# Kernel optimization log

Hardware: AMD Instinct MI355X
Metric: run time of the kernel (lower is better)

The kernel has to match this reference:

```python
import jax, jax.numpy as jnp
import numpy as np

GAMMA = 12.0
EMB_INIT = 0.05


def setup_inputs() -> dict:
    key = jax.random.key(0)
    k1, k2, k3 = jax.random.split(key, 3)
    num_chunks, chunk_size, neg_sample_size, hidden_dim = 4, 512, 256, 512
    heads = jax.random.normal(k1, (num_chunks * chunk_size, hidden_dim), dtype=jnp.float32)
    relations = jax.random.normal(k2, (num_chunks * chunk_size, hidden_dim // 2), dtype=jnp.float32)
    tails = jax.random.normal(k3, (num_chunks * neg_sample_size, hidden_dim), dtype=jnp.float32)
    return {
        "heads": heads,
        "relations": relations,
        "tails": tails,
        "num_chunks": num_chunks,
        "chunk_size": chunk_size,
        "neg_sample_size": neg_sample_size,
    }


def reference(heads, relations, tails, num_chunks, chunk_size, neg_sample_size):
    # RotatE tail-negative scoring (create_neg with neg_head=False)
    hidden_dim = heads.shape[1]
    h = hidden_dim // 2
    re_head, im_head = heads[:, :h], heads[:, h:]
    # rotate head by relation phase
    phase_rel = relations / (EMB_INIT / np.pi)
    rel_real, rel_imag = jnp.cos(phase_rel), jnp.sin(phase_rel)
    real = re_head * rel_real - im_head * rel_imag  # [nc*cs, h]
    imag = re_head * rel_imag + im_head * rel_real
    # broadcast subtract against negative tails
    tmp_r = real.reshape(num_chunks, chunk_size, 1, h)
    tmp_i = imag.reshape(num_chunks, chunk_size, 1, h)
    tails4 = tails.reshape(num_chunks, 1, neg_sample_size, hidden_dim)
    t_r, t_i = tails4[..., :h], tails4[..., h:]
    dr = tmp_r - t_r  # [nc, cs, ns, h]
    di = tmp_i - t_i
    score = jnp.sqrt(dr * dr + di * di).sum(-1)  # [nc, cs, ns]
    return GAMMA - score
```

## Files before the change

kernel.cpp:

```cpp
#include <hip/hip_runtime.h>

#define NC 4
#define CS 512
#define NS 256
#define HD 512
#define H  256
#define GAMMA_F 12.0f
#define PHASE_SCALE 62.83185307179586477f

#define TI 32
#define TJ 32
#define KT 32

__global__ __launch_bounds__(256) void score_kernel(
    const float* __restrict__ heads,
    const float* __restrict__ relations,
    const float* __restrict__ tails,
    float* __restrict__ out)
{
    __shared__ float hr[TI][KT + 1];
    __shared__ float hi_[TI][KT + 1];
    __shared__ float tr[TJ][KT + 1];
    __shared__ float ti_[TJ][KT + 1];

    int bid = blockIdx.x;
    int c = bid >> 7;
    int rem = bid & 127;
    int hTile = rem >> 3;
    int tTile = rem & 7;
    int hBase = c * CS + hTile * TI;
    int tBase = c * NS + tTile * TJ;

    int tid = threadIdx.x;
    int tx = tid & 15;
    int ty = tid >> 4;

    int lr = tid >> 3;
    int lk = (tid & 7) * 4;

    float acc00 = 0.f, acc01 = 0.f, acc10 = 0.f, acc11 = 0.f;

    for (int k0 = 0; k0 < H; k0 += KT) {
        const float* hp = heads + (size_t)(hBase + lr) * HD + k0 + lk;
        float4 hre = *reinterpret_cast<const float4*>(hp);
        float4 him = *reinterpret_cast<const float4*>(hp + H);
        float4 rel = *reinterpret_cast<const float4*>(
            relations + (size_t)(hBase + lr) * H + k0 + lk);
        const float* tp = tails + (size_t)(tBase + lr) * HD + k0 + lk;
        float4 tre = *reinterpret_cast<const float4*>(tp);
        float4 tim = *reinterpret_cast<const float4*>(tp + H);

        __syncthreads();

        {
            float s, cc;
            __sincosf(rel.x * PHASE_SCALE, &s, &cc);
            hr[lr][lk + 0] = hre.x * cc - him.x * s;
            hi_[lr][lk + 0] = hre.x * s + him.x * cc;
            __sincosf(rel.y * PHASE_SCALE, &s, &cc);
            hr[lr][lk + 1] = hre.y * cc - him.y * s;
            hi_[lr][lk + 1] = hre.y * s + him.y * cc;
            __sincosf(rel.z * PHASE_SCALE, &s, &cc);
            hr[lr][lk + 2] = hre.z * cc - him.z * s;
            hi_[lr][lk + 2] = hre.z * s + him.z * cc;
            __sincosf(rel.w * PHASE_SCALE, &s, &cc);
            hr[lr][lk + 3] = hre.w * cc - him.w * s;
            hi_[lr][lk + 3] = hre.w * s + him.w * cc;
        }
        tr[lr][lk + 0] = tre.x;  ti_[lr][lk + 0] = tim.x;
        tr[lr][lk + 1] = tre.y;  ti_[lr][lk + 1] = tim.y;
        tr[lr][lk + 2] = tre.z;  ti_[lr][lk + 2] = tim.z;
        tr[lr][lk + 3] = tre.w;  ti_[lr][lk + 3] = tim.w;

        __syncthreads();

        #pragma unroll
        for (int kk = 0; kk < KT; ++kk) {
            float h0r = hr[ty][kk],      h0i = hi_[ty][kk];
            float h1r = hr[ty + 16][kk], h1i = hi_[ty + 16][kk];
            float t0r = tr[tx][kk],      t0i = ti_[tx][kk];
            float t1r = tr[tx + 16][kk], t1i = ti_[tx + 16][kk];

            float dr, di;
            dr = h0r - t0r; di = h0i - t0i;
            acc00 += __builtin_amdgcn_sqrtf(dr * dr + di * di);
            dr = h0r - t1r; di = h0i - t1i;
            acc01 += __builtin_amdgcn_sqrtf(dr * dr + di * di);
            dr = h1r - t0r; di = h1i - t0i;
            acc10 += __builtin_amdgcn_sqrtf(dr * dr + di * di);
            dr = h1r - t1r; di = h1i - t1i;
            acc11 += __builtin_amdgcn_sqrtf(dr * dr + di * di);
        }
    }

    int i0 = hTile * TI + ty;
    int j0 = tTile * TJ + tx;
    size_t base = (size_t)c * CS * NS;
    out[base + (size_t)(i0)      * NS + j0]      = GAMMA_F - acc00;
    out[base + (size_t)(i0)      * NS + j0 + 16] = GAMMA_F - acc01;
    out[base + (size_t)(i0 + 16) * NS + j0]      = GAMMA_F - acc10;
    out[base + (size_t)(i0 + 16) * NS + j0 + 16] = GAMMA_F - acc11;
}

extern "C" void kernel_launch(void* const* d_in, const int* in_sizes, int n_in,
                              void* d_out, int out_size, void* d_ws, size_t ws_size,
                              hipStream_t stream) {
    (void)in_sizes; (void)n_in; (void)d_ws; (void)ws_size; (void)out_size;
    const float* heads = (const float*)d_in[0];
    const float* rels  = (const float*)d_in[1];
    const float* tails = (const float*)d_in[2];

    score_kernel<<<512, 256, 0, stream>>>(heads, rels, tails, (float*)d_out);
}
```

Before: 101.7 us.

## Use 64x64 register tiles with split-K over hidden dim and atomic accumulation

New measurement: 98.82 us. 1.03x faster.

```diff
diff --git a/kernel.cpp b/kernel.cpp
--- a/kernel.cpp
+++ b/kernel.cpp
@@ -8,45 +8,51 @@
 #define GAMMA_F 12.0f
 #define PHASE_SCALE 62.83185307179586477f
 
-#define TI 32
-#define TJ 32
-#define KT 32
+#define KT 16
 
-__global__ __launch_bounds__(256) void score_kernel(
+__global__ __launch_bounds__(256, 2) void score_kernel(
     const float* __restrict__ heads,
     const float* __restrict__ relations,
     const float* __restrict__ tails,
     float* __restrict__ out)
 {
-    __shared__ float hr[TI][KT + 1];
-    __shared__ float hi_[TI][KT + 1];
-    __shared__ float tr[TJ][KT + 1];
-    __shared__ float ti_[TJ][KT + 1];
+    __shared__ float2 sh[64][KT + 1];
+    __shared__ float2 st[64][KT + 1];
 
     int bid = blockIdx.x;
-    int c = bid >> 7;
-    int rem = bid & 127;
-    int hTile = rem >> 3;
-    int tTile = rem & 7;
-    int hBase = c * CS + hTile * TI;
-    int tBase = c * NS + tTile * TJ;
+    int c    = bid >> 7;
+    int rem  = bid & 127;
+    int ks   = rem >> 5;
+    int rem2 = rem & 31;
+    int hT   = rem2 >> 2;
+    int tT   = rem2 & 3;
+
+    int hBase = c * CS + hT * 64;
+    int tBase = c * NS + tT * 64;
+    int kSlice = ks * 64;
 
     int tid = threadIdx.x;
     int tx = tid & 15;
     int ty = tid >> 4;
 
-    int lr = tid >> 3;
-    int lk = (tid & 7) * 4;
+    int srow = tid >> 2;
+    int sk   = (tid & 3) * 4;
 
-    float acc00 = 0.f, acc01 = 0.f, acc10 = 0.f, acc11 = 0.f;
+    float acc[4][4];
+    #pragma unroll
+    for (int m = 0; m < 4; ++m)
+        #pragma unroll
+        for (int n = 0; n < 4; ++n) acc[m][n] = 0.f;
 
-    for (int k0 = 0; k0 < H; k0 += KT) {
-        const float* hp = heads + (size_t)(hBase + lr) * HD + k0 + lk;
+    for (int r = 0; r < 64 / KT; ++r) {
+        int kBase = kSlice + r * KT;
+
+        const float* hp = heads + (size_t)(hBase + srow) * HD + kBase + sk;
         float4 hre = *reinterpret_cast<const float4*>(hp);
         float4 him = *reinterpret_cast<const float4*>(hp + H);
         float4 rel = *reinterpret_cast<const float4*>(
-            relations + (size_t)(hBase + lr) * H + k0 + lk);
-        const float* tp = tails + (size_t)(tBase + lr) * HD + k0 + lk;
+            relations + (size_t)(hBase + srow) * H + kBase + sk);
+        const float* tp = tails + (size_t)(tBase + srow) * HD + kBase + sk;
         float4 tre = *reinterpret_cast<const float4*>(tp);
         float4 tim = *reinterpret_cast<const float4*>(tp + H);
 
@@ -55,60 +61,70 @@
         {
             float s, cc;
             __sincosf(rel.x * PHASE_SCALE, &s, &cc);
-            hr[lr][lk + 0] = hre.x * cc - him.x * s;
-            hi_[lr][lk + 0] = hre.x * s + him.x * cc;
+            sh[srow][sk + 0] = make_float2(hre.x * cc - him.x * s,
+                                           hre.x * s + him.x * cc);
             __sincosf(rel.y * PHASE_SCALE, &s, &cc);
-            hr[lr][lk + 1] = hre.y * cc - him.y * s;
-            hi_[lr][lk + 1] = hre.y * s + him.y * cc;
+            sh[srow][sk + 1] = make_float2(hre.y * cc - him.y * s,
+                                           hre.y * s + him.y * cc);
             __sincosf(rel.z * PHASE_SCALE, &s, &cc);
-            hr[lr][lk + 2] = hre.z * cc - him.z * s;
-            hi_[lr][lk + 2] = hre.z * s + him.z * cc;
+            sh[srow][sk + 2] = make_float2(hre.z * cc - him.z * s,
+                                           hre.z * s + him.z * cc);
             __sincosf(rel.w * PHASE_SCALE, &s, &cc);
-            hr[lr][lk + 3] = hre.w * cc - him.w * s;
-            hi_[lr][lk + 3] = hre.w * s + him.w * cc;
+            sh[srow][sk + 3] = make_float2(hre.w * cc - him.w * s,
+                                           hre.w * s + him.w * cc);
         }
-        tr[lr][lk + 0] = tre.x;  ti_[lr][lk + 0] = tim.x;
-        tr[lr][lk + 1] = tre.y;  ti_[lr][lk + 1] = tim.y;
-        tr[lr][lk + 2] = tre.z;  ti_[lr][lk + 2] = tim.z;
-        tr[lr][lk + 3] = tre.w;  ti_[lr][lk + 3] = tim.w;
+        st[srow][sk + 0] = make_float2(tre.x, tim.x);
+        st[srow][sk + 1] = make_float2(tre.y, tim.y);
+        st[srow][sk + 2] = make_float2(tre.z, tim.z);
+        st[srow][sk + 3] = make_float2(tre.w, tim.w);
 
         __syncthreads();
 
         #pragma unroll
         for (int kk = 0; kk < KT; ++kk) {
-            float h0r = hr[ty][kk],      h0i = hi_[ty][kk];
-            float h1r = hr[ty + 16][kk], h1i = hi_[ty + 16][kk];
-            float t0r = tr[tx][kk],      t0i = ti_[tx][kk];
-            float t1r = tr[tx + 16][kk], t1i = ti_[tx + 16][kk];
-
-            float dr, di;
-            dr = h0r - t0r; di = h0i - t0i;
-            acc00 += __builtin_amdgcn_sqrtf(dr * dr + di * di);
-            dr = h0r - t1r; di = h0i - t1i;
-            acc01 += __builtin_amdgcn_sqrtf(dr * dr + di * di);
-            dr = h1r - t0r; di = h1i - t0i;
-            acc10 += __builtin_amdgcn_sqrtf(dr * dr + di * di);
-            dr = h1r - t1r; di = h1i - t1i;
-            acc11 += __builtin_amdgcn_sqrtf(dr * dr + di * di);
+            float2 h0 = sh[ty     ][kk];
+            float2 h1 = sh[ty + 16][kk];
+            float2 h2 = sh[ty + 32][kk];
+            float2 h3 = sh[ty + 48][kk];
+            float2 t0 = st[tx     ][kk];
+            float2 t1 = st[tx + 16][kk];
+            float2 t2 = st[tx + 32][kk];
+            float2 t3 = st[tx + 48][kk];
+            float2 hv[4] = {h0, h1, h2, h3};
+            float2 tv[4] = {t0, t1, t2, t3};
+            #pragma unroll
+            for (int m = 0; m < 4; ++m) {
+                #pragma unroll
+                for (int n = 0; n < 4; ++n) {
+                    float dr = hv[m].x - tv[n].x;
+                    float di = hv[m].y - tv[n].y;
+                    acc[m][n] += __builtin_amdgcn_sqrtf(dr * dr + di * di);
+                }
+            }
         }
     }
 
-    int i0 = hTile * TI + ty;
-    int j0 = tTile * TJ + tx;
-    size_t base = (size_t)c * CS * NS;
-    out[base + (size_t)(i0)      * NS + j0]      = GAMMA_F - acc00;
-    out[base + (size_t)(i0)      * NS + j0 + 16] = GAMMA_F - acc01;
-    out[base + (size_t)(i0 + 16) * NS + j0]      = GAMMA_F - acc10;
-    out[base + (size_t)(i0 + 16) * NS + j0 + 16] = GAMMA_F - acc11;
+    float base_add = (ks == 0) ? GAMMA_F : 0.f;
+    size_t cbase = (size_t)c * CS * NS;
+    #pragma unroll
+    for (int m = 0; m < 4; ++m) {
+        int i0 = hT * 64 + ty + 16 * m;
+        #pragma unroll
+        for (int n = 0; n < 4; ++n) {
+            int j0 = tT * 64 + tx + 16 * n;
+            atomicAdd(&out[cbase + (size_t)i0 * NS + j0], base_add - acc[m][n]);
+        }
+    }
 }
 
 extern "C" void kernel_launch(void* const* d_in, const int* in_sizes, int n_in,
                               void* d_out, int out_size, void* d_ws, size_t ws_size,
                               hipStream_t stream) {
-    (void)in_sizes; (void)n_in; (void)d_ws; (void)ws_size; (void)out_size;
+    (void)in_sizes; (void)n_in; (void)d_ws; (void)ws_size;
     const float* heads = (const float*)d_in[0];
     const float* rels  = (const float*)d_in[1];
     const float* tails = (const float*)d_in[2];
 
+    hipMemsetAsync(d_out, 0, (size_t)out_size * sizeof(float), stream);
     score_kernel<<<512, 256, 0, stream>>>(heads, rels, tails, (float*)d_out);
 }
```
